# Kernel optimization log

Hardware: AMD Instinct MI355X
Metric: run time of the kernel (lower is better)

Reference implementation:

```python
import jax, jax.numpy as jnp
import numpy as np

N = 4
TMAX = 20
EPS = 1e-06
POST_MULT = 2.0


def setup_inputs() -> dict:
    key = jax.random.key(0)
    ks = jax.random.split(key, 8)
    T, C = 8192, 1024
    return {
        "x": jax.random.normal(ks[0], (T, N, C), dtype=jnp.float32),
        "f_out": jax.random.normal(ks[1], (T, C), dtype=jnp.float32),
        "mix": jax.random.normal(ks[2], (T, 2 * N + N * N), dtype=jnp.float32),
        "invr": jax.random.uniform(ks[3], (T,), dtype=jnp.float32),
        "alpha_pre": jax.random.uniform(ks[4], (1,), dtype=jnp.float32),
        "alpha_post": jax.random.uniform(ks[5], (1,), dtype=jnp.float32),
        "alpha_res": jax.random.uniform(ks[6], (1,), dtype=jnp.float32),
        "bias": jax.random.normal(ks[7], (2 * N + N * N,), dtype=jnp.float32),
    }


def _sinkhorn(r):
    # r: (T, N, N) logits. Row-softmax exp, then TMAX row/col normalizations.
    r = jnp.exp(r - jnp.max(r, axis=-1, keepdims=True))
    def body(_, r):
        r = r / (jnp.sum(r, axis=-1, keepdims=True) + EPS)  # row normalize
        r = r / (jnp.sum(r, axis=-2, keepdims=True) + EPS)  # col normalize
        return r
    return jax.lax.fori_loop(0, TMAX, body, r)


def reference(x, f_out, mix, invr, alpha_pre, alpha_post, alpha_res, bias):
    T = mix.shape[0]
    s = mix * invr[:, None]  # (T, 24)
    h_pre = jax.nn.sigmoid(s[:, :N] * alpha_pre + bias[:N])                      # (T, N)
    h_post = jax.nn.sigmoid(s[:, N:2 * N] * alpha_post + bias[N:2 * N]) * POST_MULT  # (T, N)
    r = (s[:, 2 * N:] * alpha_res + bias[2 * N:]).reshape(T, N, N)
    h_res = _sinkhorn(r)  # (T, N, N), doubly-normalized mixing matrix
    # pre-aggregate the N residual streams into one (input to the wrapped sublayer)
    y_pre = jnp.einsum("tn,tnc->tc", h_pre, x)
    # residual remix + gated sublayer output broadcast back to N streams
    out = jnp.einsum("tji,tic->tjc", h_res, x) + h_post[:, :, None] * f_out[:, None, :]
    return y_pre, out
```

## Files before the change

kernel.cpp:

```cpp
#include <hip/hip_runtime.h>
#include <math.h>

#define NN 4
#define TMAX 20
#define EPS 1e-6f
#define POST_MULT 2.0f

__global__ __launch_bounds__(256) void fused_mhc_kernel(
    const float* __restrict__ x,
    const float* __restrict__ f_out,
    const float* __restrict__ mix,
    const float* __restrict__ invr,
    const float* __restrict__ alpha_pre,
    const float* __restrict__ alpha_post,
    const float* __restrict__ alpha_res,
    const float* __restrict__ bias,
    float* __restrict__ y_pre,
    float* __restrict__ out,
    int C)
{
    const int t = blockIdx.x;
    const int tid = threadIdx.x;

    __shared__ float sh_pre[NN];
    __shared__ float sh_post[NN];
    __shared__ float sh_res[NN * NN];

    if (tid < 64) {
        const int lane = tid;
        const float ir = invr[t];
        if (lane < 16) {
            float r = mix[t * 24 + 8 + lane] * ir * alpha_res[0] + bias[8 + lane];
            float m = r;
            m = fmaxf(m, __shfl_xor(m, 1));
            m = fmaxf(m, __shfl_xor(m, 2));
            r = __expf(r - m);
            #pragma unroll
            for (int it = 0; it < TMAX; ++it) {
                float rs = r;
                rs += __shfl_xor(rs, 1);
                rs += __shfl_xor(rs, 2);
                r = r / (rs + EPS);
                float cs = r;
                cs += __shfl_xor(cs, 4);
                cs += __shfl_xor(cs, 8);
                r = r / (cs + EPS);
            }
            sh_res[lane] = r;
        } else if (lane < 24) {
            const int idx = lane - 16;
            const float a = (idx < NN) ? alpha_pre[0] : alpha_post[0];
            const float z = mix[t * 24 + idx] * ir * a + bias[idx];
            const float sg = 1.0f / (1.0f + __expf(-z));
            if (idx < NN) sh_pre[idx] = sg;
            else          sh_post[idx - NN] = sg * POST_MULT;
        }
    }
    __syncthreads();

    const float hp0 = sh_pre[0], hp1 = sh_pre[1], hp2 = sh_pre[2], hp3 = sh_pre[3];

    const int NV = C >> 2;
    const float4* xv4 = (const float4*)(x + (size_t)t * NN * C);
    const float4* fv4 = (const float4*)(f_out + (size_t)t * C);
    float4* yp4 = (float4*)(y_pre + (size_t)t * C);
    float4* o4  = (float4*)(out + (size_t)t * NN * C);

    for (int v = tid; v < NV; v += blockDim.x) {
        float4 xv[NN];
        #pragma unroll
        for (int n = 0; n < NN; ++n) xv[n] = xv4[n * NV + v];
        const float4 fv = fv4[v];

        float4 yv;
        yv.x = hp0 * xv[0].x; yv.y = hp0 * xv[0].y; yv.z = hp0 * xv[0].z; yv.w = hp0 * xv[0].w;
        yv.x = fmaf(hp1, xv[1].x, yv.x); yv.y = fmaf(hp1, xv[1].y, yv.y);
        yv.z = fmaf(hp1, xv[1].z, yv.z); yv.w = fmaf(hp1, xv[1].w, yv.w);
        yv.x = fmaf(hp2, xv[2].x, yv.x); yv.y = fmaf(hp2, xv[2].y, yv.y);
        yv.z = fmaf(hp2, xv[2].z, yv.z); yv.w = fmaf(hp2, xv[2].w, yv.w);
        yv.x = fmaf(hp3, xv[3].x, yv.x); yv.y = fmaf(hp3, xv[3].y, yv.y);
        yv.z = fmaf(hp3, xv[3].z, yv.z); yv.w = fmaf(hp3, xv[3].w, yv.w);
        yp4[v] = yv;

        #pragma unroll
        for (int j = 0; j < NN; ++j) {
            const float hq = sh_post[j];
            float4 ov;
            ov.x = hq * fv.x; ov.y = hq * fv.y; ov.z = hq * fv.z; ov.w = hq * fv.w;
            #pragma unroll
            for (int i = 0; i < NN; ++i) {
                const float h = sh_res[j * NN + i];
                ov.x = fmaf(h, xv[i].x, ov.x);
                ov.y = fmaf(h, xv[i].y, ov.y);
                ov.z = fmaf(h, xv[i].z, ov.z);
                ov.w = fmaf(h, xv[i].w, ov.w);
            }
            o4[j * NV + v] = ov;
        }
    }
}

extern "C" void kernel_launch(void* const* d_in, const int* in_sizes, int n_in,
                              void* d_out, int out_size, void* d_ws, size_t ws_size,
                              hipStream_t stream) {
    const float* x          = (const float*)d_in[0];
    const float* f_out      = (const float*)d_in[1];
    const float* mix        = (const float*)d_in[2];
    const float* invr       = (const float*)d_in[3];
    const float* alpha_pre  = (const float*)d_in[4];
    const float* alpha_post = (const float*)d_in[5];
    const float* alpha_res  = (const float*)d_in[6];
    const float* bias       = (const float*)d_in[7];

    const int T = in_sizes[3];
    const int C = in_sizes[1] / T;

    float* y_pre = (float*)d_out;
    float* out   = (float*)d_out + (size_t)T * C;

    fused_mhc_kernel<<<T, 256, 0, stream>>>(x, f_out, mix, invr,
                                            alpha_pre, alpha_post, alpha_res,
                                            bias, y_pre, out, C);
}
```

Baseline: 304.6 us.

## Split Sinkhorn coefficient computation into separate kernel and use nontemporal stores

Moves the per-token sigmoid and Sinkhorn coefficient computation out of the streaming kernel into a dense pre-pass kernel. That kernel packs 16 tokens per block and writes the coefficients to workspace. The streaming kernel then reads the coefficients directly, with no shared memory or __syncthreads, so the serial 20-iteration Sinkhorn latency no longer stalls each bandwidth-bound block. Output stores become nontemporal vector stores to reduce cache pollution. The cost is an extra kernel launch and a small workspace round trip.

```diff
diff --git a/kernel.cpp b/kernel.cpp
--- a/kernel.cpp
+++ b/kernel.cpp
@@ -6,96 +6,95 @@
 #define EPS 1e-6f
 #define POST_MULT 2.0f
 
-__global__ __launch_bounds__(256) void fused_mhc_kernel(
-    const float* __restrict__ x,
-    const float* __restrict__ f_out,
+typedef float vfloat4 __attribute__((ext_vector_type(4)));
+
+__global__ __launch_bounds__(256) void coeff_kernel(
     const float* __restrict__ mix,
     const float* __restrict__ invr,
     const float* __restrict__ alpha_pre,
     const float* __restrict__ alpha_post,
     const float* __restrict__ alpha_res,
     const float* __restrict__ bias,
+    float* __restrict__ coeffs,
+    int T)
+{
+    const int gtid = blockIdx.x * blockDim.x + threadIdx.x;
+    const int t    = gtid >> 4;
+    const int lane = gtid & 15;
+    if (t >= T) return;
+
+    const float ir = invr[t];
+
+    float r = mix[t * 24 + 8 + lane] * ir * alpha_res[0] + bias[8 + lane];
+    float m = r;
+    m = fmaxf(m, __shfl_xor(m, 1));
+    m = fmaxf(m, __shfl_xor(m, 2));
+    r = __expf(r - m);
+    #pragma unroll
+    for (int it = 0; it < TMAX; ++it) {
+        float rs = r;
+        rs += __shfl_xor(rs, 1);
+        rs += __shfl_xor(rs, 2);
+        r = r / (rs + EPS);
+        float cs = r;
+        cs += __shfl_xor(cs, 4);
+        cs += __shfl_xor(cs, 8);
+        r = r / (cs + EPS);
+    }
+    coeffs[t * 24 + 8 + lane] = r;
+
+    if (lane < 8) {
+        const float a = (lane < NN) ? alpha_pre[0] : alpha_post[0];
+        const float z = mix[t * 24 + lane] * ir * a + bias[lane];
+        float sg = 1.0f / (1.0f + __expf(-z));
+        if (lane >= NN) sg *= POST_MULT;
+        coeffs[t * 24 + lane] = sg;
+    }
+}
+
+__global__ __launch_bounds__(256) void stream_kernel(
+    const float* __restrict__ x,
+    const float* __restrict__ f_out,
+    const float* __restrict__ coeffs,
     float* __restrict__ y_pre,
     float* __restrict__ out,
     int C)
 {
-    const int t = blockIdx.x;
+    const int t   = blockIdx.x;
     const int tid = threadIdx.x;
 
-    __shared__ float sh_pre[NN];
-    __shared__ float sh_post[NN];
-    __shared__ float sh_res[NN * NN];
-
-    if (tid < 64) {
-        const int lane = tid;
-        const float ir = invr[t];
-        if (lane < 16) {
-            float r = mix[t * 24 + 8 + lane] * ir * alpha_res[0] + bias[8 + lane];
-            float m = r;
-            m = fmaxf(m, __shfl_xor(m, 1));
-            m = fmaxf(m, __shfl_xor(m, 2));
-            r = __expf(r - m);
-            #pragma unroll
-            for (int it = 0; it < TMAX; ++it) {
-                float rs = r;
-                rs += __shfl_xor(rs, 1);
-                rs += __shfl_xor(rs, 2);
-                r = r / (rs + EPS);
-                float cs = r;
-                cs += __shfl_xor(cs, 4);
-                cs += __shfl_xor(cs, 8);
-                r = r / (cs + EPS);
-            }
-            sh_res[lane] = r;
-        } else if (lane < 24) {
-            const int idx = lane - 16;
-            const float a = (idx < NN) ? alpha_pre[0] : alpha_post[0];
-            const float z = mix[t * 24 + idx] * ir * a + bias[idx];
-            const float sg = 1.0f / (1.0f + __expf(-z));
-            if (idx < NN) sh_pre[idx] = sg;
-            else          sh_post[idx - NN] = sg * POST_MULT;
-        }
-    }
-    __syncthreads();
-
-    const float hp0 = sh_pre[0], hp1 = sh_pre[1], hp2 = sh_pre[2], hp3 = sh_pre[3];
+    const float* cf = coeffs + (size_t)t * 24;
+    const float hp0 = cf[0], hp1 = cf[1], hp2 = cf[2], hp3 = cf[3];
+    const float hq0 = cf[4], hq1 = cf[5], hq2 = cf[6], hq3 = cf[7];
+    float hr[NN][NN];
+    #pragma unroll
+    for (int j = 0; j < NN; ++j)
+        #pragma unroll
+        for (int i = 0; i < NN; ++i)
+            hr[j][i] = cf[8 + j * 4 + i];
 
     const int NV = C >> 2;
-    const float4* xv4 = (const float4*)(x + (size_t)t * NN * C);
-    const float4* fv4 = (const float4*)(f_out + (size_t)t * C);
-    float4* yp4 = (float4*)(y_pre + (size_t)t * C);
-    float4* o4  = (float4*)(out + (size_t)t * NN * C);
+    const vfloat4* xv4 = (const vfloat4*)(x + (size_t)t * NN * C);
+    const vfloat4* fv4 = (const vfloat4*)(f_out + (size_t)t * C);
+    vfloat4* yp4 = (vfloat4*)(y_pre + (size_t)t * C);
+    vfloat4* o4  = (vfloat4*)(out + (size_t)t * NN * C);
 
     for (int v = tid; v < NV; v += blockDim.x) {
-        float4 xv[NN];
+        vfloat4 xv[NN];
         #pragma unroll
         for (int n = 0; n < NN; ++n) xv[n] = xv4[n * NV + v];
-        const float4 fv = fv4[v];
+        const vfloat4 fv = fv4[v];
 
-        float4 yv;
-        yv.x = hp0 * xv[0].x; yv.y = hp0 * xv[0].y; yv.z = hp0 * xv[0].z; yv.w = hp0 * xv[0].w;
-        yv.x = fmaf(hp1, xv[1].x, yv.x); yv.y = fmaf(hp1, xv[1].y, yv.y);
-        yv.z = fmaf(hp1, xv[1].z, yv.z); yv.w = fmaf(hp1, xv[1].w, yv.w);
-        yv.x = fmaf(hp2, xv[2].x, yv.x); yv.y = fmaf(hp2, xv[2].y, yv.y);
-        yv.z = fmaf(hp2, xv[2].z, yv.z); yv.w = fmaf(hp2, xv[2].w, yv.w);
-        yv.x = fmaf(hp3, xv[3].x, yv.x); yv.y = fmaf(hp3, xv[3].y, yv.y);
-        yv.z = fmaf(hp3, xv[3].z, yv.z); yv.w = fmaf(hp3, xv[3].w, yv.w);
-        yp4[v] = yv;
+        vfloat4 yv = hp0 * xv[0] + hp1 * xv[1] + hp2 * xv[2] + hp3 * xv[3];
+        __builtin_nontemporal_store(yv, &yp4[v]);
 
+        const float hq[NN] = {hq0, hq1, hq2, hq3};
         #pragma unroll
         for (int j = 0; j < NN; ++j) {
-            const float hq = sh_post[j];
-            float4 ov;
-            ov.x = hq * fv.x; ov.y = hq * fv.y; ov.z = hq * fv.z; ov.w = hq * fv.w;
+            vfloat4 ov = hq[j] * fv;
             #pragma unroll
-            for (int i = 0; i < NN; ++i) {
-                const float h = sh_res[j * NN + i];
-                ov.x = fmaf(h, xv[i].x, ov.x);
-                ov.y = fmaf(h, xv[i].y, ov.y);
-                ov.z = fmaf(h, xv[i].z, ov.z);
-                ov.w = fmaf(h, xv[i].w, ov.w);
-            }
-            o4[j * NV + v] = ov;
+            for (int i = 0; i < NN; ++i) ov += hr[j][i] * xv[i];
+            __builtin_nontemporal_store(ov, &o4[j * NV + v]);
         }
     }
 }
@@ -117,8 +116,10 @@
 
     float* y_pre = (float*)d_out;
     float* out   = (float*)d_out + (size_t)T * C;
+    float* coeffs = (float*)d_ws;
 
-    fused_mhc_kernel<<<T, 256, 0, stream>>>(x, f_out, mix, invr,
-                                            alpha_pre, alpha_post, alpha_res,
-                                            bias, y_pre, out, C);
+    const int grid1 = (T * 16 + 255) / 256;
+    coeff_kernel<<<grid1, 256, 0, stream>>>(mix, invr, alpha_pre, alpha_post,
+                                            alpha_res, bias, coeffs, T);
+    stream_kernel<<<T, 256, 0, stream>>>(x, f_out, coeffs, y_pre, out, C);
 }
```

Measured after the change: 304.1 us. About the same (-0.2%).
